# Kernel optimization log

Hardware: AMD Instinct MI355X
Metric: run time of the kernel (lower is better)

Reference implementation:

```python
import jax, jax.numpy as jnp
import numpy as np
import math

D_MODEL = 512
SLOPE = 0.5  # slope_init, not trainable


def setup_inputs() -> dict:
    key = jax.random.key(0)
    k1, k2, k3, k4 = jax.random.split(key, 4)
    B, S, D = 4, 4096, D_MODEL
    x = jax.random.normal(k1, (B, S, D), dtype=jnp.float32)
    # nn.Linear(d, d): weight is [d, d]; query_key weight used as x @ W (no transpose, bias unused)
    lim = 1.0 / math.sqrt(D)
    W_qk = jax.random.uniform(k2, (D, D), jnp.float32, -lim, lim)
    W_v = jax.random.uniform(k3, (D, D), jnp.float32, -lim, lim)
    b_v = jax.random.uniform(k4, (D,), jnp.float32, -lim, lim)
    return {"x": x, "W_qk": W_qk, "W_v": W_v, "b_v": b_v}


def reference(x, W_qk, W_v, b_v):
    B, S, D = x.shape
    scale = 1.0 / math.sqrt(D)
    # scores[b,i,j] = (x @ W_qk @ x^T) * scale   (torch: x @ weight @ x.transpose)
    scores = jnp.einsum('bid,de,bje->bij', x, W_qk, x) * scale
    # ALiBi bias: (j - i) * slope
    i = jnp.arange(S, dtype=x.dtype)[:, None]
    j = jnp.arange(S, dtype=x.dtype)[None, :]
    scores = scores + (j - i) * jnp.asarray(SLOPE, x.dtype)
    # causal mask: strict upper triangle -> -inf
    causal = j > i  # [S, S] bool
    scores = jnp.where(causal, -jnp.inf, scores)
    attn = jax.nn.softmax(scores, axis=-1)
    # value_linear: x @ W_v^T + b_v (standard nn.Linear)
    v = jnp.einsum('bjd,ed->bje', x, W_v) + b_v
    return jnp.einsum('bij,bje->bie', attn, v)
```

## Files before the change

### kernel.cpp

```cpp
#include <hip/hip_runtime.h>
#include <math.h>

#define D_MODEL 512
#define SEQ     4096
#define BATCH   4
#define BS      (BATCH * SEQ)

typedef __attribute__((ext_vector_type(8))) short  short8;
typedef __attribute__((ext_vector_type(4))) float  float4v;

#define GAS __attribute__((address_space(1)))
#define LAS __attribute__((address_space(3)))

__device__ __forceinline__ void gld_lds16(const void* g, void* l) {
  __builtin_amdgcn_global_load_lds((const GAS unsigned int*)g,
                                   (LAS unsigned int*)l, 16, 0, 0);
}

__device__ __forceinline__ unsigned short bf16r(float f) {
  unsigned int u = __builtin_bit_cast(unsigned int, f);
  u += 0x7fffu + ((u >> 16) & 1u);
  return (unsigned short)(u >> 16);
}

__device__ __forceinline__ uint4 pack8(float4 a, float4 b) {
  uint4 o;
  o.x = bf16r(a.x) | ((unsigned)bf16r(a.y) << 16);
  o.y = bf16r(a.z) | ((unsigned)bf16r(a.w) << 16);
  o.z = bf16r(b.x) | ((unsigned)bf16r(b.y) << 16);
  o.w = bf16r(b.z) | ((unsigned)bf16r(b.w) << 16);
  return o;
}

__global__ __launch_bounds__(256) void cvt_w(const float* __restrict__ Wqk,
                                             unsigned short* __restrict__ Wqkt,
                                             const float* __restrict__ Wv,
                                             unsigned short* __restrict__ Wvb,
                                             const float* __restrict__ x,
                                             unsigned short* __restrict__ xb) {
  if (blockIdx.x < 64) {
    __shared__ float tile[64][65];
    const int bx = blockIdx.x & 7;
    const int by = blockIdx.x >> 3;
    const int tx = threadIdx.x & 63;
    const int ty = threadIdx.x >> 6;
    for (int r = ty; r < 64; r += 4)
      tile[r][tx] = Wqk[(size_t)(by * 64 + r) * D_MODEL + bx * 64 + tx];
    __syncthreads();
    for (int r = ty; r < 64; r += 4)
      Wqkt[(size_t)(bx * 64 + r) * D_MODEL + by * 64 + tx] = bf16r(tile[tx][r]);
  } else if (blockIdx.x < 192) {
    const int idx = ((blockIdx.x - 64) * 256 + threadIdx.x) * 8;
    const float4 a = *(const float4*)(Wv + idx);
    const float4 b = *(const float4*)(Wv + idx + 4);
    *(uint4*)(Wvb + idx) = pack8(a, b);
  } else {
    const size_t idx = ((size_t)(blockIdx.x - 192) * 256 + threadIdx.x) * 8;
    const float4 a = *(const float4*)(x + idx);
    const float4 b = *(const float4*)(x + idx + 4);
    *(uint4*)(xb + idx) = pack8(a, b);
  }
}

template <bool QP>
__device__ __forceinline__ void gemm_path(const unsigned short* __restrict__ xb,
                                          const unsigned short* __restrict__ Wgt,
                                          const float* __restrict__ bias,
                                          unsigned short* __restrict__ C,
                                          int a0, float scale,
                                          unsigned short* Ws, unsigned short* As) {
  const int t    = threadIdx.x;
  const int w    = t >> 6;
  const int lane = t & 63;
  const int q    = lane >> 4;
  const int c    = lane & 15;
  const int wbase = w * 128;
  const int sw   = c & 7;

  constexpr int NI = QP ? 8 : 4;
  constexpr int NJ = QP ? 4 : 8;

  float4v acc[NI][NJ];
#pragma unroll
  for (int i = 0; i < NI; ++i)
#pragma unroll
    for (int j = 0; j < NJ; ++j) acc[i][j] = (float4v){0.f, 0.f, 0.f, 0.f};

  for (int k0 = 0; k0 < D_MODEL; k0 += 64) {
#pragma unroll
    for (int it = 0; it < 16; ++it) {
      const int idx = it * 256 + t;
      const int r   = idx >> 3;
      const int s   = idx & 7;
      gld_lds16(Wgt + (size_t)r * D_MODEL + k0 + ((s ^ (r & 7)) << 3),
                &Ws[idx * 8]);
    }
#pragma unroll
    for (int it = 0; it < 2; ++it) {
      const int idx = it * 256 + t;
      const int r   = idx >> 3;
      const int s   = idx & 7;
      gld_lds16(xb + (size_t)(a0 + r) * D_MODEL + k0 + ((s ^ (r & 7)) << 3),
                &As[idx * 8]);
    }
    __syncthreads();

#pragma unroll
    for (int kc = 0; kc < 2; ++kc) {
      const int slot = ((kc * 4 + q) ^ sw) * 8;
      short8 af[NI], bf[NJ];
#pragma unroll
      for (int i = 0; i < NI; ++i) {
        const unsigned short* src = QP ? &Ws[(wbase + i * 16 + c) * 64 + slot]
                                       : &As[(i * 16 + c) * 64 + slot];
        af[i] = *(const short8*)src;
      }
#pragma unroll
      for (int j = 0; j < NJ; ++j) {
        const unsigned short* src = QP ? &As[(j * 16 + c) * 64 + slot]
                                       : &Ws[(wbase + j * 16 + c) * 64 + slot];
        bf[j] = *(const short8*)src;
      }
#pragma unroll
      for (int i = 0; i < NI; ++i)
#pragma unroll
        for (int j = 0; j < NJ; ++j)
          acc[i][j] = __builtin_amdgcn_mfma_f32_16x16x32_bf16(af[i], bf[j], acc[i][j], 0, 0, 0);
    }
    __syncthreads();
  }

  if (QP) {
#pragma unroll
    for (int j = 0; j < NJ; ++j) {
      const size_t row = a0 + j * 16 + c;
#pragma unroll
      for (int i = 0; i < NI; ++i) {
        uint2 pkt;
        pkt.x = (unsigned)bf16r(scale * acc[i][j][0]) |
                ((unsigned)bf16r(scale * acc[i][j][1]) << 16);
        pkt.y = (unsigned)bf16r(scale * acc[i][j][2]) |
                ((unsigned)bf16r(scale * acc[i][j][3]) << 16);
        *(uint2*)&C[row * D_MODEL + wbase + i * 16 + 4 * q] = pkt;
      }
    }
  } else {
#pragma unroll
    for (int j = 0; j < NJ; ++j) {
      const int dim = wbase + j * 16 + c;
      const float bvv = bias[dim];
#pragma unroll
      for (int i = 0; i < NI; ++i) {
        const int key = a0 + i * 16 + 4 * q;
        uint2 pkt;
        pkt.x = (unsigned)bf16r(acc[i][j][0] + bvv) |
                ((unsigned)bf16r(acc[i][j][1] + bvv) << 16);
        pkt.y = (unsigned)bf16r(acc[i][j][2] + bvv) |
                ((unsigned)bf16r(acc[i][j][3] + bvv) << 16);
        *(uint2*)&C[(size_t)dim * BS + key] = pkt;
      }
    }
  }
}

__global__ __launch_bounds__(256, 2) void qv_gemm(const unsigned short* __restrict__ xb,
                                                  const unsigned short* __restrict__ Wqkt,
                                                  const unsigned short* __restrict__ Wvb,
                                                  const float* __restrict__ bv,
                                                  unsigned short* __restrict__ Qb,
                                                  unsigned short* __restrict__ Vt,
                                                  float scale) {
  __shared__ unsigned short Ws[512 * 64];
  __shared__ unsigned short As[64 * 64];
  if (blockIdx.x < 256)
    gemm_path<true>(xb, Wqkt, nullptr, Qb, blockIdx.x * 64, scale, Ws, As);
  else
    gemm_path<false>(xb, Wvb, bv, Vt, (blockIdx.x - 256) * 64, 1.0f, Ws, As);
}

__global__ __launch_bounds__(128) void attn_tile(const unsigned short* __restrict__ Q,
                                                 const unsigned short* __restrict__ Kx,
                                                 const unsigned short* __restrict__ Vt,
                                                 float* __restrict__ out) {
  constexpr int PLD = 72;
  __shared__ unsigned short pls[16 * PLD];
  __shared__ float lm[2][16], ls[2][16];

  const int t    = threadIdx.x;
  const int h    = t >> 6;
  const int lane = t & 63;
  const int q    = lane >> 4;
  const int c    = lane & 15;

  const int tile = ((blockIdx.x & 7) << 7) + (blockIdx.x >> 3);
  const int r0   = tile << 4;
  const int b    = r0 >> 12;
  const int i0   = r0 & (SEQ - 1);
  const int jb   = i0 - 48;

  short8 qf[16];
  {
    const unsigned short* qp = Q + (size_t)(r0 + c) * D_MODEL + q * 8;
#pragma unroll
    for (int ch = 0; ch < 16; ++ch) qf[ch] = *(const short8*)(qp + ch * 32);
  }

  float4v sacc[2];
  sacc[0] = (float4v){0.f, 0.f, 0.f, 0.f};
  sacc[1] = (float4v){0.f, 0.f, 0.f, 0.f};
#pragma unroll
  for (int s = 0; s < 2; ++s) {
    const int sj = 2 * h + s;
    if (jb + 16 * sj + 15 < 0) continue;
    int krow = jb + 16 * sj + c;
    if (krow < 0) krow = 0;
    const unsigned short* kr = Kx + ((size_t)(b << 12) + krow) * D_MODEL + q * 8;
    float4v sv = sacc[s];
#pragma unroll
    for (int ch = 0; ch < 16; ++ch)
      sv = __builtin_amdgcn_mfma_f32_16x16x32_bf16(qf[ch], *(const short8*)(kr + ch * 32), sv, 0, 0, 0);
    sacc[s] = sv;
  }

  const unsigned short* vbase = Vt + (size_t)(h * 256 + c) * BS + (b << 12);
  const bool ch0 = (jb + 31 >= 0);
  short8 vf0[16];
  if (ch0) {
    int kk = jb + q * 8;
    if (kk < 0) kk = 0;
    const unsigned short* vb = vbase + kk;
#pragma unroll
    for (int dt = 0; dt < 16; ++dt) vf0[dt] = *(const short8*)(vb + (size_t)dt * 16 * BS);
  }

  float tmax[4] = {-1e30f, -1e30f, -1e30f, -1e30f};
#pragma unroll
  for (int s = 0; s < 2; ++s)
#pragma unroll
    for (int tt = 0; tt < 4; ++tt) {
      const int jl = jb + 16 * (2 * h + s) + c;
      const int il = i0 + 4 * q + tt;
      float sv = sacc[s][tt];
      sv = (jl < 0 || jl > il) ? -1e30f : sv + 0.5f * (float)(jl - il);
      sacc[s][tt] = sv;
      tmax[tt] = fmaxf(tmax[tt], sv);
    }
#pragma unroll
  for (int tt = 0; tt < 4; ++tt) {
    float v = tmax[tt];
    v = fmaxf(v, __shfl_xor(v, 1, 64));
    v = fmaxf(v, __shfl_xor(v, 2, 64));
    v = fmaxf(v, __shfl_xor(v, 4, 64));
    v = fmaxf(v, __shfl_xor(v, 8, 64));
    tmax[tt] = v;
  }
  if (c == 0) {
#pragma unroll
    for (int tt = 0; tt < 4; ++tt) lm[h][4 * q + tt] = tmax[tt];
  }
  __syncthreads();

  float m[4];
#pragma unroll
  for (int tt = 0; tt < 4; ++tt)
    m[tt] = fmaxf(lm[0][4 * q + tt], lm[1][4 * q + tt]);

  float rsum[4] = {0.f, 0.f, 0.f, 0.f};
#pragma unroll
  for (int s = 0; s < 2; ++s)
#pragma unroll
    for (int tt = 0; tt < 4; ++tt) {
      const float p = __expf(sacc[s][tt] - m[tt]);
      rsum[tt] += p;
      pls[(4 * q + tt) * PLD + (2 * h + s) * 16 + c] = bf16r(p);
    }
#pragma unroll
  for (int tt = 0; tt < 4; ++tt) {
    float v = rsum[tt];
    v += __shfl_xor(v, 1, 64);
    v += __shfl_xor(v, 2, 64);
    v += __shfl_xor(v, 4, 64);
    v += __shfl_xor(v, 8, 64);
    rsum[tt] = v;
  }
  if (c == 0) {
#pragma unroll
    for (int tt = 0; tt < 4; ++tt) ls[h][4 * q + tt] = rsum[tt];
  }
  __syncthreads();

  float l[4];
#pragma unroll
  for (int tt = 0; tt < 4; ++tt)
    l[tt] = ls[0][4 * q + tt] + ls[1][4 * q + tt];

  float4v oacc[16];
#pragma unroll
  for (int dt = 0; dt < 16; ++dt) oacc[dt] = (float4v){0.f, 0.f, 0.f, 0.f};

  if (ch0) {
    const short8 pa = *(const short8*)&pls[c * PLD + q * 8];
#pragma unroll
    for (int dt = 0; dt < 16; ++dt)
      oacc[dt] = __builtin_amdgcn_mfma_f32_16x16x32_bf16(pa, vf0[dt], oacc[dt], 0, 0, 0);
  }
  {
    const short8 pa = *(const short8*)&pls[c * PLD + 32 + q * 8];
    int kk = jb + 32 + q * 8;
    if (kk < 0) kk = 0;
    const unsigned short* vb = vbase + kk;
#pragma unroll
    for (int dt = 0; dt < 16; ++dt) {
      const short8 vf = *(const short8*)(vb + (size_t)dt * 16 * BS);
      oacc[dt] = __builtin_amdgcn_mfma_f32_16x16x32_bf16(pa, vf, oacc[dt], 0, 0, 0);
    }
  }

  float inv[4];
#pragma unroll
  for (int tt = 0; tt < 4; ++tt) inv[tt] = 1.0f / l[tt];
#pragma unroll
  for (int dt = 0; dt < 16; ++dt)
#pragma unroll
    for (int tt = 0; tt < 4; ++tt)
      out[(size_t)(r0 + 4 * q + tt) * D_MODEL + h * 256 + dt * 16 + c] =
          oacc[dt][tt] * inv[tt];
}

extern "C" void kernel_launch(void* const* d_in, const int* in_sizes, int n_in,
                              void* d_out, int out_size, void* d_ws,
                              size_t ws_size, hipStream_t stream) {
  const float* x   = (const float*)d_in[0];
  const float* Wqk = (const float*)d_in[1];
  const float* Wv  = (const float*)d_in[2];
  const float* bv  = (const float*)d_in[3];
  float* out = (float*)d_out;

  unsigned short* xb   = (unsigned short*)d_ws;
  unsigned short* Qb   = xb + (size_t)BS * D_MODEL;
  unsigned short* Vt   = Qb + (size_t)BS * D_MODEL;
  unsigned short* Wqkt = Vt + (size_t)BS * D_MODEL;
  unsigned short* Wvb  = Wqkt + (size_t)D_MODEL * D_MODEL;

  const float scale = 1.0f / sqrtf((float)D_MODEL);

  cvt_w<<<dim3(192 + (BS * D_MODEL / 2048)), dim3(256), 0, stream>>>(Wqk, Wqkt, Wv, Wvb, x, xb);
  qv_gemm<<<dim3(512), dim3(256), 0, stream>>>(xb, Wqkt, Wvb, bv, Qb, Vt, scale);
  attn_tile<<<dim3(BS / 16), dim3(128), 0, stream>>>(Qb, xb, Vt, out);
}
```

Measured before the change: 134.2 us.

## Fuse x bf16 conversion into projection GEMM and stage epilogue stores through LDS

Drops the separate pass that converts x to bf16. The Q/V projection GEMM now loads fp32 x directly, converts it in registers, writes the swizzled tile to LDS, and the Q-path blocks also emit the bf16 copy of x that the attention kernel uses as keys. The Q and V epilogues now stage results in shared memory (with padded strides) and write them out as coalesced 16-byte rows instead of scattered 8-byte stores. In exchange, x tiles now go through synchronous register loads instead of async global-to-LDS loads, and each x tile is read as fp32 twice (once by the Q path, once by the V path).

```diff
diff --git a/kernel.cpp b/kernel.cpp
--- a/kernel.cpp
+++ b/kernel.cpp
@@ -35,9 +35,7 @@
 __global__ __launch_bounds__(256) void cvt_w(const float* __restrict__ Wqk,
                                              unsigned short* __restrict__ Wqkt,
                                              const float* __restrict__ Wv,
-                                             unsigned short* __restrict__ Wvb,
-                                             const float* __restrict__ x,
-                                             unsigned short* __restrict__ xb) {
+                                             unsigned short* __restrict__ Wvb) {
   if (blockIdx.x < 64) {
     __shared__ float tile[64][65];
     const int bx = blockIdx.x & 7;
@@ -49,26 +47,25 @@
     __syncthreads();
     for (int r = ty; r < 64; r += 4)
       Wqkt[(size_t)(bx * 64 + r) * D_MODEL + by * 64 + tx] = bf16r(tile[tx][r]);
-  } else if (blockIdx.x < 192) {
+  } else {
     const int idx = ((blockIdx.x - 64) * 256 + threadIdx.x) * 8;
     const float4 a = *(const float4*)(Wv + idx);
     const float4 b = *(const float4*)(Wv + idx + 4);
     *(uint4*)(Wvb + idx) = pack8(a, b);
-  } else {
-    const size_t idx = ((size_t)(blockIdx.x - 192) * 256 + threadIdx.x) * 8;
-    const float4 a = *(const float4*)(x + idx);
-    const float4 b = *(const float4*)(x + idx + 4);
-    *(uint4*)(xb + idx) = pack8(a, b);
   }
 }
 
 template <bool QP>
-__device__ __forceinline__ void gemm_path(const unsigned short* __restrict__ xb,
+__device__ __forceinline__ void gemm_path(const float* __restrict__ x,
                                           const unsigned short* __restrict__ Wgt,
                                           const float* __restrict__ bias,
+                                          unsigned short* __restrict__ xb,
                                           unsigned short* __restrict__ C,
                                           int a0, float scale,
-                                          unsigned short* Ws, unsigned short* As) {
+                                          unsigned short* smem) {
+  unsigned short* Ws = smem;
+  unsigned short* As = smem + 32768;
+
   const int t    = threadIdx.x;
   const int w    = t >> 6;
   const int lane = t & 63;
@@ -77,6 +74,9 @@
   const int wbase = w * 128;
   const int sw   = c & 7;
 
+  const int arow = t >> 2;
+  const int acb  = (t & 3) * 16;
+
   constexpr int NI = QP ? 8 : 4;
   constexpr int NJ = QP ? 4 : 8;
 
@@ -95,13 +95,23 @@
       gld_lds16(Wgt + (size_t)r * D_MODEL + k0 + ((s ^ (r & 7)) << 3),
                 &Ws[idx * 8]);
     }
-#pragma unroll
-    for (int it = 0; it < 2; ++it) {
-      const int idx = it * 256 + t;
-      const int r   = idx >> 3;
-      const int s   = idx & 7;
-      gld_lds16(xb + (size_t)(a0 + r) * D_MODEL + k0 + ((s ^ (r & 7)) << 3),
-                &As[idx * 8]);
+    {
+      const float* xg = x + (size_t)(a0 + arow) * D_MODEL + k0 + acb;
+      const float4 f0 = *(const float4*)(xg + 0);
+      const float4 f1 = *(const float4*)(xg + 4);
+      const float4 f2 = *(const float4*)(xg + 8);
+      const float4 f3 = *(const float4*)(xg + 12);
+      const uint4 u0 = pack8(f0, f1);
+      const uint4 u1 = pack8(f2, f3);
+      const int s0 = (t & 3) * 2;
+      const int rk = arow & 7;
+      *(uint4*)&As[arow * 64 + ((s0 ^ rk) << 3)]       = u0;
+      *(uint4*)&As[arow * 64 + (((s0 + 1) ^ rk) << 3)] = u1;
+      if (QP) {
+        unsigned short* xo = xb + (size_t)(a0 + arow) * D_MODEL + k0 + acb;
+        *(uint4*)xo       = u0;
+        *(uint4*)(xo + 8) = u1;
+      }
     }
     __syncthreads();
 
@@ -131,9 +141,10 @@
   }
 
   if (QP) {
+    constexpr int LD = 520;
 #pragma unroll
     for (int j = 0; j < NJ; ++j) {
-      const size_t row = a0 + j * 16 + c;
+      const int row = j * 16 + c;
 #pragma unroll
       for (int i = 0; i < NI; ++i) {
         uint2 pkt;
@@ -141,41 +152,59 @@
                 ((unsigned)bf16r(scale * acc[i][j][1]) << 16);
         pkt.y = (unsigned)bf16r(scale * acc[i][j][2]) |
                 ((unsigned)bf16r(scale * acc[i][j][3]) << 16);
-        *(uint2*)&C[row * D_MODEL + wbase + i * 16 + 4 * q] = pkt;
-      }
+        *(uint2*)&smem[row * LD + wbase + i * 16 + 4 * q] = pkt;
+      }
+    }
+    __syncthreads();
+#pragma unroll
+    for (int it = 0; it < 16; ++it) {
+      const int idx = it * 256 + t;
+      const int row = idx >> 6;
+      const int ch  = idx & 63;
+      *(uint4*)&C[(size_t)(a0 + row) * D_MODEL + ch * 8] =
+          *(const uint4*)&smem[row * LD + ch * 8];
     }
   } else {
+    constexpr int LD = 72;
 #pragma unroll
     for (int j = 0; j < NJ; ++j) {
       const int dim = wbase + j * 16 + c;
       const float bvv = bias[dim];
 #pragma unroll
       for (int i = 0; i < NI; ++i) {
-        const int key = a0 + i * 16 + 4 * q;
         uint2 pkt;
         pkt.x = (unsigned)bf16r(acc[i][j][0] + bvv) |
                 ((unsigned)bf16r(acc[i][j][1] + bvv) << 16);
         pkt.y = (unsigned)bf16r(acc[i][j][2] + bvv) |
                 ((unsigned)bf16r(acc[i][j][3] + bvv) << 16);
-        *(uint2*)&C[(size_t)dim * BS + key] = pkt;
-      }
-    }
-  }
-}
-
-__global__ __launch_bounds__(256, 2) void qv_gemm(const unsigned short* __restrict__ xb,
+        *(uint2*)&smem[dim * LD + i * 16 + 4 * q] = pkt;
+      }
+    }
+    __syncthreads();
+#pragma unroll
+    for (int it = 0; it < 16; ++it) {
+      const int idx = it * 256 + t;
+      const int dim = idx >> 3;
+      const int ch  = idx & 7;
+      *(uint4*)&C[(size_t)dim * BS + a0 + ch * 8] =
+          *(const uint4*)&smem[dim * LD + ch * 8];
+    }
+  }
+}
+
+__global__ __launch_bounds__(256, 2) void qv_gemm(const float* __restrict__ x,
                                                   const unsigned short* __restrict__ Wqkt,
                                                   const unsigned short* __restrict__ Wvb,
                                                   const float* __restrict__ bv,
+                                                  unsigned short* __restrict__ xb,
                                                   unsigned short* __restrict__ Qb,
                                                   unsigned short* __restrict__ Vt,
                                                   float scale) {
-  __shared__ unsigned short Ws[512 * 64];
-  __shared__ unsigned short As[64 * 64];
+  __shared__ unsigned short smem[36864];
   if (blockIdx.x < 256)
-    gemm_path<true>(xb, Wqkt, nullptr, Qb, blockIdx.x * 64, scale, Ws, As);
+    gemm_path<true>(x, Wqkt, nullptr, xb, Qb, blockIdx.x * 64, scale, smem);
   else
-    gemm_path<false>(xb, Wvb, bv, Vt, (blockIdx.x - 256) * 64, 1.0f, Ws, As);
+    gemm_path<false>(x, Wvb, bv, nullptr, Vt, (blockIdx.x - 256) * 64, 1.0f, smem);
 }
 
 __global__ __launch_bounds__(128) void attn_tile(const unsigned short* __restrict__ Q,
@@ -344,7 +373,7 @@
 
   const float scale = 1.0f / sqrtf((float)D_MODEL);
 
-  cvt_w<<<dim3(192 + (BS * D_MODEL / 2048)), dim3(256), 0, stream>>>(Wqk, Wqkt, Wv, Wvb, x, xb);
-  qv_gemm<<<dim3(512), dim3(256), 0, stream>>>(xb, Wqkt, Wvb, bv, Qb, Vt, scale);
+  cvt_w<<<dim3(192), dim3(256), 0, stream>>>(Wqk, Wqkt, Wv, Wvb);
+  qv_gemm<<<dim3(512), dim3(256), 0, stream>>>(x, Wqkt, Wvb, bv, xb, Qb, Vt, scale);
   attn_tile<<<dim3(BS / 16), dim3(128), 0, stream>>>(Qb, xb, Vt, out);
 }
```

After: 133.2 us. About the same (-0.8%).
